# Optimization experiments

Measured on AMD Instinct MI355X. Metric: run time of the kernel, lower is better.

Reference implementation:

```python
import jax, jax.numpy as jnp
import numpy as np

IOU_THR = 0.5
SCORE_THR = 0.5
MAX_DET = 100
B, N, C = 16, 25200, 80


def setup_inputs() -> dict:
    key = jax.random.key(0)
    k1, k2, k3 = jax.random.split(key, 3)
    return {
        "boxes_xywh": jax.random.uniform(k1, (B, N, 4), dtype=jnp.float32),
        "objectness": jax.random.uniform(k2, (B, N, 1), dtype=jnp.float32),
        "class_prob": jax.random.uniform(k3, (B, N, C), dtype=jnp.float32),
    }


def _xywh_to_corners(b):
    x, y, w, h = jnp.split(b, 4, axis=-1)
    return jnp.concatenate([x - w / 2, y - h / 2, x + w / 2, y + h / 2], axis=-1)


def _broadcast_iou(box, boxes):
    # box [4], boxes [N,4] in x1,y1,x2,y2
    lt = jnp.maximum(box[:2], boxes[:, :2])
    rb = jnp.minimum(box[2:], boxes[:, 2:])
    wh = jnp.clip(rb - lt, 0.0)
    inter = wh[:, 0] * wh[:, 1]
    a1 = (box[2] - box[0]) * (box[3] - box[1])
    a2 = (boxes[:, 2] - boxes[:, 0]) * (boxes[:, 3] - boxes[:, 1])
    return inter / (a1 + a2 - inter + 1e-9)


def _nms_single(cand):
    # cand: [N, 4+1+C] rows = (x1,y1,x2,y2, score, class_probs...)
    n, d = cand.shape
    scores = cand[:, 4]
    active0 = scores >= SCORE_THR

    def body(i, state):
        active, out, count = state
        masked = jnp.where(active, scores, -jnp.inf)
        best = jnp.argmax(masked)
        valid = jnp.any(active)
        best_box = cand[best]
        out = out.at[i].set(jnp.where(valid, best_box, out[i]))
        count = count + valid.astype(jnp.int32)
        iou = _broadcast_iou(best_box[:4], cand[:, :4])
        keep = active & (iou <= IOU_THR)
        keep = keep.at[best].set(False)
        active = jnp.where(valid, keep, active)
        return active, out, count

    out0 = jnp.zeros((MAX_DET, d), cand.dtype)
    _, out, count = jax.lax.fori_loop(0, MAX_DET, body, (active0, out0, jnp.int32(0)))
    return out, count


def reference(boxes_xywh, objectness, class_prob):
    corners = _xywh_to_corners(boxes_xywh)  # [B,N,4]
    combined = jnp.concatenate([corners, objectness, class_prob], axis=-1)  # [B,N,5+C]
    final_result, count = jax.vmap(_nms_single)(combined)  # [B,MAX_DET,5+C], [B]
    nms_boxes = final_result[..., 0:4]
    nms_scores = final_result[..., 4:5]
    nms_classes = final_result[..., 5:]
    valid_count = count.astype(jnp.int32)[:, None]  # [B,1]
    return nms_boxes, nms_scores, nms_classes, valid_count
```

## Files before the change

### kernel.cpp

```cpp
#include <hip/hip_runtime.h>

#define NBOX    25200
#define NQ4     6300
#define NBATCH  16
#define NCLS    80
#define MAXDET  100
#define NBUCKET 1024
#define CAP     13824
#define SCORE_THR 0.5f
#define IOU_THR   0.5f
#define NGROUP  16

__device__ __forceinline__ void mk_corners(float x, float y, float w, float h,
                                           float& x1, float& y1, float& x2, float& y2) {
#pragma clang fp contract(off)
    float hw = w * 0.5f;
    float hh = h * 0.5f;
    x1 = x - hw; y1 = y - hh; x2 = x + hw; y2 = y + hh;
}

__device__ __forceinline__ float areaf(float x1, float y1, float x2, float y2) {
#pragma clang fp contract(off)
    return (x2 - x1) * (y2 - y1);
}

__device__ __forceinline__ bool iou_gt(float kx1, float ky1, float kx2, float ky2, float ka,
                                       float cx1, float cy1, float cx2, float cy2, float ca) {
#pragma clang fp contract(off)
    float lx = fmaxf(kx1, cx1);
    float ly = fmaxf(ky1, cy1);
    float rx = fminf(kx2, cx2);
    float ry = fminf(ky2, cy2);
    float w  = fmaxf(rx - lx, 0.0f);
    float h  = fmaxf(ry - ly, 0.0f);
    float inter = w * h;
    float denom = ka + ca - inter + 1e-9f;
    return (inter / denom) > IOU_THR;
}

__device__ __forceinline__ float readlane_f(float v, int j) {
    return __uint_as_float((unsigned)__builtin_amdgcn_readlane((int)__float_as_uint(v), j));
}

__device__ __forceinline__ unsigned score_key(float s) {
    return __float_as_uint(s) - 0x3F000000u;
}

__global__ __launch_bounds__(1024)
void nms_kernel(const float* __restrict__ boxes_xywh,
                const float* __restrict__ objectness,
                const float* __restrict__ class_prob,
                float* __restrict__ out) {
    __shared__ unsigned s_hist[NBUCKET];
    __shared__ unsigned s_start[NBUCKET];
    __shared__ unsigned s_a[CAP];
    __shared__ unsigned s_b[CAP];
    __shared__ float4   s_kbox[MAXDET];
    __shared__ float    s_karea[MAXDET];
    __shared__ unsigned s_kept_idx[MAXDET];
    __shared__ unsigned s_wsum[16];
    __shared__ unsigned s_woff[16];
    __shared__ int      s_count;

    const int b = blockIdx.x;
    const int t = threadIdx.x;
    const int w = t >> 6;
    const int l = t & 63;
    const float* obj = objectness + (size_t)b * NBOX;
    const float* bx  = boxes_xywh + (size_t)b * NBOX * 4;

    float4 r[7];
#pragma unroll
    for (int i = 0; i < 7; ++i) {
        int n4 = t + (i << 10);
        if (n4 < NQ4) r[i] = *(const float4*)(obj + n4 * 4);
    }

    s_hist[t] = 0u;
    __syncthreads();
#pragma unroll
    for (int i = 0; i < 7; ++i) {
        int n4 = t + (i << 10);
        if (n4 < NQ4) {
            float sv[4] = {r[i].x, r[i].y, r[i].z, r[i].w};
#pragma unroll
            for (int u = 0; u < 4; ++u) {
                if (sv[u] >= SCORE_THR) {
                    unsigned bkt = score_key(sv[u]) >> 13;
                    if (bkt > 1023u) bkt = 1023u;
                    atomicAdd(&s_hist[bkt], 1u);
                }
            }
        }
    }
    __syncthreads();

    {
        unsigned f = s_hist[1023 - t];
        unsigned v = f;
#pragma unroll
        for (int off = 1; off < 64; off <<= 1) {
            unsigned u = (unsigned)__shfl_up((int)v, off);
            if (l >= off) v += u;
        }
        if (l == 63) s_wsum[w] = v;
        __syncthreads();
        if (t < 64) {
            unsigned x = (t < 16) ? s_wsum[t] : 0u;
            unsigned y = x;
#pragma unroll
            for (int off = 1; off < 16; off <<= 1) {
                unsigned u = (unsigned)__shfl_up((int)y, off);
                if (t >= off) y += u;
            }
            if (t < 16) s_woff[t] = y - x;
        }
        __syncthreads();
        s_start[1023 - t] = v - f + s_woff[w];
    }
    if (t == 0) s_count = 0;
    __syncthreads();

#pragma unroll
    for (int i = 0; i < 7; ++i) {
        int n4 = t + (i << 10);
        if (n4 < NQ4) {
            float sv[4] = {r[i].x, r[i].y, r[i].z, r[i].w};
#pragma unroll
            for (int u = 0; u < 4; ++u) {
                if (sv[u] >= SCORE_THR) {
                    unsigned ekey = score_key(sv[u]);
                    unsigned bkt  = ekey >> 13;
                    if (bkt > 1023u) bkt = 1023u;
                    int n = n4 * 4 + u;
                    unsigned pos = atomicAdd(&s_start[bkt], 1u);
                    if (pos < CAP)
                        s_a[pos] = ((ekey & 0x1FFFu) << 18) | (0x3FFFFu - (unsigned)n);
                }
            }
        }
    }
    __syncthreads();

    auto sort_bucket = [&](int bkt) {
        unsigned h = s_hist[bkt];
        if (h == 0u) return;
        unsigned end = s_start[bkt];
        unsigned hi  = (end > CAP) ? CAP : end;
        unsigned lo  = (end >= h) ? end - h : 0u;
        if (lo > hi) lo = hi;
        unsigned sz = hi - lo;
        if (sz == 0u) return;
        if (sz <= 64u) {
            unsigned v = (l < (int)sz) ? s_a[lo + (unsigned)l] : 0u;
            int rank = 0;
            for (unsigned j = 0; j < sz; ++j)
                rank += ((unsigned)__shfl((int)v, (int)j) > v) ? 1 : 0;
            if (l < (int)sz) s_b[lo + (unsigned)rank] = v;
        } else {
            for (unsigned bb = 0; bb < sz; bb += 64u) {
                bool valid = bb + (unsigned)l < sz;
                unsigned v = valid ? s_a[lo + bb + (unsigned)l] : 0u;
                int rank = 0;
                for (unsigned j = 0; j < sz; ++j)
                    rank += (s_a[lo + j] > v) ? 1 : 0;
                if (valid) s_b[lo + (unsigned)rank] = v;
            }
        }
    };

    for (int bkt = (1023 - 63) + w; bkt <= 1023; bkt += 16) sort_bucket(bkt);
    __syncthreads();

    int count = 0;
    for (int g = 0; g < NGROUP; ++g) {
        const int BH = 1023 - (g << 6);
        const int BL = BH - 63;

        if (w == 0) {
            unsigned glo = (g == 0) ? 0u : s_start[BH + 1];
            unsigned ghi = s_start[BL];
            if (glo > CAP) glo = CAP;
            if (ghi > CAP) ghi = CAP;

            if (glo < ghi && count < MAXDET) {
                unsigned i0, i1, i2, i3;
                float4 q0, q1, q2, q3;
                auto loadc = [&](unsigned cb, unsigned& ix, float4& q) {
                    ix = 0u; q = make_float4(0.f, 0.f, 0.f, 0.f);
                    unsigned p0 = cb + (unsigned)l;
                    if (p0 < ghi) {
                        unsigned p = s_b[p0];
                        ix = 0x3FFFFu - (p & 0x3FFFFu);
                        q = *(const float4*)(bx + (size_t)ix * 4);
                    }
                };
                loadc(glo,        i0, q0);
                loadc(glo + 64u,  i1, q1);
                loadc(glo + 128u, i2, q2);
                loadc(glo + 192u, i3, q3);

                for (unsigned base = glo; base < ghi && count < MAXDET; base += 64u) {
                    unsigned cidx = i0; float4 cq = q0;
                    i0 = i1; q0 = q1;
                    i1 = i2; q1 = q2;
                    i2 = i3; q2 = q3;
                    loadc(base + 256u, i3, q3);

                    int m = (int)(ghi - base); if (m > 64) m = 64;
                    float cx1, cy1, cx2, cy2;
                    mk_corners(cq.x, cq.y, cq.z, cq.w, cx1, cy1, cx2, cy2);
                    float ca = areaf(cx1, cy1, cx2, cy2);

                    bool sup = (l >= m);
                    int k = 0;
                    for (; k + 4 <= count; k += 4) {
                        float4 kb0 = s_kbox[k],     kb1 = s_kbox[k + 1];
                        float4 kb2 = s_kbox[k + 2], kb3 = s_kbox[k + 3];
                        float ka0 = s_karea[k],     ka1 = s_karea[k + 1];
                        float ka2 = s_karea[k + 2], ka3 = s_karea[k + 3];
                        sup = sup | iou_gt(kb0.x, kb0.y, kb0.z, kb0.w, ka0,
                                           cx1, cy1, cx2, cy2, ca);
                        sup = sup | iou_gt(kb1.x, kb1.y, kb1.z, kb1.w, ka1,
                                           cx1, cy1, cx2, cy2, ca);
                        sup = sup | iou_gt(kb2.x, kb2.y, kb2.z, kb2.w, ka2,
                                           cx1, cy1, cx2, cy2, ca);
                        sup = sup | iou_gt(kb3.x, kb3.y, kb3.z, kb3.w, ka3,
                                           cx1, cy1, cx2, cy2, ca);
                    }
                    for (; k < count; ++k) {
                        float4 kb = s_kbox[k];
                        sup = sup | iou_gt(kb.x, kb.y, kb.z, kb.w, s_karea[k],
                                           cx1, cy1, cx2, cy2, ca);
                    }
                    unsigned long long act = __ballot(!sup);

                    unsigned long long accmask = 0ull;
                    const int cbase = count;
                    while (act != 0ull && count < MAXDET) {
                        int j = (int)__builtin_ctzll(act);
                        accmask |= 1ull << j;
                        float bx1 = readlane_f(cx1, j), by1 = readlane_f(cy1, j);
                        float bx2 = readlane_f(cx2, j), by2 = readlane_f(cy2, j);
                        float bar = readlane_f(ca, j);
                        bool su = iou_gt(bx1, by1, bx2, by2, bar, cx1, cy1, cx2, cy2, ca);
                        ++count;
                        act &= ~(1ull << j);
                        act &= ~__ballot(su);
                    }

                    if (accmask & (1ull << l)) {
                        int slot = cbase + (int)__popcll(accmask & ((1ull << l) - 1ull));
                        s_kbox[slot] = make_float4(cx1, cy1, cx2, cy2);
                        s_karea[slot] = ca;
                        s_kept_idx[slot] = cidx;
                        float* ob = out + ((size_t)b * MAXDET + slot) * 4;
                        ob[0] = cx1; ob[1] = cy1; ob[2] = cx2; ob[3] = cy2;
                        out[NBATCH * MAXDET * 4 + b * MAXDET + slot] = obj[cidx];
                    }
                    __asm__ volatile("s_waitcnt lgkmcnt(0)" ::: "memory");
                }
            }
            if (l == 0) s_count = count;
        } else if (g + 1 < NGROUP) {
            const int BH2 = BH - 64, BL2 = BH2 - 63;
            for (int bkt = BL2 + (w - 1); bkt <= BH2; bkt += 15) sort_bucket(bkt);
        }
        __syncthreads();
        if (s_count >= MAXDET) break;
    }

    const int cf = s_count;
    for (int e = t; e < MAXDET * 4; e += 1024) {
        if ((e >> 2) >= cf) out[(size_t)b * MAXDET * 4 + e] = 0.0f;
    }
    for (int i = t; i < MAXDET; i += 1024) {
        if (i >= cf) out[NBATCH * MAXDET * 4 + b * MAXDET + i] = 0.0f;
    }
    const float* cp = class_prob + (size_t)b * NBOX * NCLS;
    float* oc = out + NBATCH * MAXDET * 5 + (size_t)b * MAXDET * NCLS;
    float4* oc4 = (float4*)oc;
    const int NQC = NCLS / 4;
    const int nq = cf * NQC;
    for (int e4 = t; e4 < nq; e4 += 1024) {
        int i  = e4 / NQC;
        int c4 = e4 - i * NQC;
        oc4[e4] = *((const float4*)(cp + (size_t)s_kept_idx[i] * NCLS) + c4);
    }
    for (int e4 = t + nq; e4 < MAXDET * NQC; e4 += 1024)
        oc4[e4] = make_float4(0.0f, 0.0f, 0.0f, 0.0f);
    if (t == 0)
        out[NBATCH * MAXDET * 5 + NBATCH * MAXDET * NCLS + b] = (float)cf;
}

extern "C" void kernel_launch(void* const* d_in, const int* in_sizes, int n_in,
                              void* d_out, int out_size, void* d_ws, size_t ws_size,
                              hipStream_t stream) {
    const float* boxes = (const float*)d_in[0];
    const float* objn  = (const float*)d_in[1];
    const float* clsp  = (const float*)d_in[2];
    float* out = (float*)d_out;
    nms_kernel<<<dim3(NBATCH), dim3(1024), 0, stream>>>(boxes, objn, clsp, out);
}
```

Baseline: 199.4 us.

## Offload candidate-vs-kept IoU suppression to helper wavefronts with published masks

Other wavefronts now run alongside the single serial NMS wavefront. After finishing their bucket sorts they spin, and for each upcoming 64-candidate chunk they precompute suppression against the boxes kept so far. They publish a ballot mask and a watermark to shared memory via acquire/release atomics, so the main wave only checks kept boxes added after the watermark. This aims to shorten the serial critical path. The cost is spin-polling wavefronts competing for issue slots and LDS bandwidth, plus added synchronisation complexity.

```diff
diff --git a/kernel.cpp b/kernel.cpp
--- a/kernel.cpp
+++ b/kernel.cpp
@@ -10,6 +10,7 @@
 #define SCORE_THR 0.5f
 #define IOU_THR   0.5f
 #define NGROUP  16
+#define MAXCH   30
 
 __device__ __forceinline__ void mk_corners(float x, float y, float w, float h,
                                            float& x1, float& y1, float& x2, float& y2) {
@@ -61,6 +62,11 @@
     __shared__ unsigned s_wsum[16];
     __shared__ unsigned s_woff[16];
     __shared__ int      s_count;
+    __shared__ unsigned           s_pub_wm[MAXCH];
+    __shared__ unsigned long long s_pub_mask[MAXCH];
+    __shared__ int      s_livecnt;
+    __shared__ int      s_groupdone;
+    __shared__ int      s_chunkpos;
 
     const int b = blockIdx.x;
     const int t = threadIdx.x;
@@ -177,12 +183,21 @@
         const int BH = 1023 - (g << 6);
         const int BL = BH - 63;
 
+        unsigned glo = (g == 0) ? 0u : s_start[BH + 1];
+        unsigned ghi = s_start[BL];
+        if (glo > CAP) glo = CAP;
+        if (ghi > CAP) ghi = CAP;
+        int nch = 0;
+        if (ghi > glo) {
+            unsigned c = (ghi - glo + 63u) >> 6;
+            nch = (c > (unsigned)MAXCH) ? MAXCH : (int)c;
+        }
+
+        if (t < MAXCH) { s_pub_wm[t] = 0u; s_pub_mask[t] = 0ull; }
+        if (t == 0) { s_groupdone = 0; s_chunkpos = 0; s_livecnt = s_count; }
+        __syncthreads();
+
         if (w == 0) {
-            unsigned glo = (g == 0) ? 0u : s_start[BH + 1];
-            unsigned ghi = s_start[BL];
-            if (glo > CAP) glo = CAP;
-            if (ghi > CAP) ghi = CAP;
-
             if (glo < ghi && count < MAXDET) {
                 unsigned i0, i1, i2, i3;
                 float4 q0, q1, q2, q3;
@@ -212,8 +227,16 @@
                     mk_corners(cq.x, cq.y, cq.z, cq.w, cx1, cy1, cx2, cy2);
                     float ca = areaf(cx1, cy1, cx2, cy2);
 
-                    bool sup = (l >= m);
-                    int k = 0;
+                    const int ci = (int)((base - glo) >> 6);
+                    int wm = 0;
+                    unsigned long long hm = 0ull;
+                    if (ci < nch) {
+                        wm = (int)__hip_atomic_load(&s_pub_wm[ci], __ATOMIC_ACQUIRE,
+                                                    __HIP_MEMORY_SCOPE_WORKGROUP);
+                        hm = *(volatile unsigned long long*)&s_pub_mask[ci];
+                    }
+                    bool sup = (l >= m) | (((hm >> l) & 1ull) != 0ull);
+                    int k = wm;
                     for (; k + 4 <= count; k += 4) {
                         float4 kb0 = s_kbox[k],     kb1 = s_kbox[k + 1];
                         float4 kb2 = s_kbox[k + 2], kb3 = s_kbox[k + 3];
@@ -259,12 +282,74 @@
                         out[NBATCH * MAXDET * 4 + b * MAXDET + slot] = obj[cidx];
                     }
                     __asm__ volatile("s_waitcnt lgkmcnt(0)" ::: "memory");
+                    if (l == 0) {
+                        *(volatile int*)&s_chunkpos = ci + 1;
+                        __hip_atomic_store(&s_livecnt, count, __ATOMIC_RELEASE,
+                                           __HIP_MEMORY_SCOPE_WORKGROUP);
+                    }
                 }
             }
-            if (l == 0) s_count = count;
-        } else if (g + 1 < NGROUP) {
-            const int BH2 = BH - 64, BL2 = BH2 - 63;
-            for (int bkt = BL2 + (w - 1); bkt <= BH2; bkt += 15) sort_bucket(bkt);
+            if (l == 0) {
+                s_count = count;
+                __hip_atomic_store(&s_groupdone, 1, __ATOMIC_RELEASE,
+                                   __HIP_MEMORY_SCOPE_WORKGROUP);
+            }
+        } else {
+            if (g + 1 < NGROUP) {
+                const int BH2 = BH - 64, BL2 = BH2 - 63;
+                for (int bkt = BL2 + (w - 1); bkt <= BH2; bkt += 15) sort_bucket(bkt);
+            }
+            float hx1[2], hy1[2], hx2[2], hy2[2], hca[2];
+            bool  hsup[2];
+            bool  hgath[2] = {false, false};
+            int   hwm[2]   = {0, 0};
+            while (true) {
+                if (__hip_atomic_load(&s_groupdone, __ATOMIC_ACQUIRE,
+                                      __HIP_MEMORY_SCOPE_WORKGROUP)) break;
+                int lc   = __hip_atomic_load(&s_livecnt, __ATOMIC_ACQUIRE,
+                                             __HIP_MEMORY_SCOPE_WORKGROUP);
+                int cpos = *(volatile int*)&s_chunkpos;
+                bool any = false;
+#pragma unroll
+                for (int q = 0; q < 2; ++q) {
+                    int ci = (w - 1) + q * 15;
+                    if (ci >= nch || ci < cpos) continue;
+                    if (lc > hwm[q]) {
+                        if (!hgath[q]) {
+                            unsigned p0 = glo + ((unsigned)ci << 6) + (unsigned)l;
+                            bool valid = p0 < ghi;
+                            float4 qq = make_float4(0.f, 0.f, 0.f, 0.f);
+                            if (valid) {
+                                unsigned p = s_b[p0];
+                                unsigned ix = 0x3FFFFu - (p & 0x3FFFFu);
+                                qq = *(const float4*)(bx + (size_t)ix * 4);
+                            }
+                            mk_corners(qq.x, qq.y, qq.z, qq.w,
+                                       hx1[q], hy1[q], hx2[q], hy2[q]);
+                            hca[q]  = areaf(hx1[q], hy1[q], hx2[q], hy2[q]);
+                            hsup[q] = !valid;
+                            hgath[q] = true;
+                        }
+                        bool sup = hsup[q];
+                        for (int kk = hwm[q]; kk < lc; ++kk) {
+                            float4 kb = s_kbox[kk];
+                            sup = sup | iou_gt(kb.x, kb.y, kb.z, kb.w, s_karea[kk],
+                                               hx1[q], hy1[q], hx2[q], hy2[q], hca[q]);
+                        }
+                        hsup[q] = sup;
+                        unsigned long long bm = __ballot(sup);
+                        if (l == 0) {
+                            *(volatile unsigned long long*)&s_pub_mask[ci] = bm;
+                            __hip_atomic_store(&s_pub_wm[ci], (unsigned)lc,
+                                               __ATOMIC_RELEASE,
+                                               __HIP_MEMORY_SCOPE_WORKGROUP);
+                        }
+                        hwm[q] = lc;
+                        any = true;
+                    }
+                }
+                if (!any) __builtin_amdgcn_s_sleep(1);
+            }
         }
         __syncthreads();
         if (s_count >= MAXDET) break;
```

New measurement: 200.1 us. Within noise of the previous version (+0.3%).
